# Kernel optimization log

Measured on AMD Instinct MI355X. Metric: run time of the kernel, lower is better.

Reference implementation:

```python
import jax, jax.numpy as jnp
import numpy as np

N = 100_000   # nodes
D = 128       # in_size == out_size
E = 800_000   # edges per etype
NE = 2        # number of edge types
H = 4         # num_heads
HD = D // H   # head size
EPS = 1e-5


def setup_inputs() -> dict:
    key = jax.random.key(0)
    ks = jax.random.split(key, 10)
    s = 0.05
    return {
        "feat": jax.random.normal(ks[0], (N, D), jnp.float32),
        "src": jax.random.randint(ks[1], (NE, E), 0, N, dtype=jnp.int32),
        "dst": jax.random.randint(ks[2], (NE, E), 0, N, dtype=jnp.int32),
        # per-etype Linear weights stored [in, out] so y = x @ W + b (torch stores transposed)
        "Wt": jax.random.normal(ks[3], (NE, D, D), jnp.float32) * s,
        "bt": jnp.zeros((NE, D), jnp.float32),
        "Kw": jax.random.normal(ks[4], (NE, D, D), jnp.float32) * s,
        "Kb": jnp.zeros((NE, D), jnp.float32),
        "Qw": jax.random.normal(ks[5], (NE, D, D), jnp.float32) * s,
        "Qb": jnp.zeros((NE, D), jnp.float32),
        "Vw": jax.random.normal(ks[6], (NE, D, D), jnp.float32) * s,
        "Vb": jnp.zeros((NE, D), jnp.float32),
        "ln_g": jnp.ones((D,), jnp.float32),
        "ln_b": jnp.zeros((D,), jnp.float32),
    }


def _attn(Wh, kw, kb, qw, qb, vw, vb):
    # per-node multi-head attention ACROSS HEADS: attn is [N, H, H] (faithful to bmm in torch code)
    k = (Wh @ kw + kb).reshape(-1, H, HD)
    q = (Wh @ qw + qb).reshape(-1, H, HD)
    v = (Wh @ vw + vb).reshape(-1, H, HD)
    scores = jnp.einsum('nhd,ngd->nhg', q, k) / np.float32(np.sqrt(HD))
    a = jax.nn.softmax(scores, axis=2)  # dropout is identity in eval
    return jnp.einsum('nhg,ngd->nhd', a, v).reshape(-1, D)


def reference(feat, src, dst, Wt, bt, Kw, Kb, Qw, Qb, Vw, Vb, ln_g, ln_b):
    h = jnp.zeros_like(feat)
    ones_e = jnp.ones((E,), feat.dtype)
    for e in range(NE):  # small fixed loop over edge types
        Wh = _attn(feat @ Wt[e] + bt[e], Kw[e], Kb[e], Qw[e], Qb[e], Vw[e], Vb[e])
        msg = Wh[src[e]]                                      # copy_u: [E, D]
        tot = jax.ops.segment_sum(msg, dst[e], num_segments=N)
        deg = jax.ops.segment_sum(ones_e, dst[e], num_segments=N)
        h = h + tot / jnp.maximum(deg, 1.0)[:, None]          # mean (0 for isolated), cross-etype 'sum'
    h = h + feat  # identity residual (in_size == out_size)
    mu = jnp.mean(h, axis=-1, keepdims=True)
    var = jnp.mean((h - mu) ** 2, axis=-1, keepdims=True)
    return (h - mu) / jnp.sqrt(var + EPS) * ln_g + ln_b  # LayerNorm; dropout identity in eval
```

## Files before the change

### kernel.cpp

```cpp
#include <hip/hip_runtime.h>
#include <hip/hip_bf16.h>
#include <stdint.h>

#define D 128
#define NET 2
#define CAP 32
#define CSTR 4
#define NB_BUILD 128

typedef __bf16 bf16x8 __attribute__((ext_vector_type(8)));
typedef float f32x4 __attribute__((ext_vector_type(4)));
typedef short s16x8 __attribute__((ext_vector_type(8)));
typedef unsigned short us16x8 __attribute__((ext_vector_type(8)));

__device__ __forceinline__ float b2f(unsigned short u) {
  return __builtin_bit_cast(float, ((uint32_t)u) << 16);
}
__device__ __forceinline__ unsigned short f2b(float f) {
  __hip_bfloat16 h = __float2bfloat16(f);
  return __builtin_bit_cast(unsigned short, h);
}

__global__ void k_combine(const float* __restrict__ Wt, const float* __restrict__ bt,
                          const float* __restrict__ Kw, const float* __restrict__ Kb,
                          const float* __restrict__ Qw, const float* __restrict__ Qb,
                          const float* __restrict__ Vw, const float* __restrict__ Vb,
                          unsigned short* __restrict__ WTc, float* __restrict__ bc) {
  int combo = blockIdx.y;
  int et = combo / 3, which = combo % 3;
  const float* W0 = Wt + (size_t)et * D * D;
  const float* W1 = ((which == 0) ? Kw : (which == 1) ? Qw : Vw) + (size_t)et * D * D;
  const float* b1 = ((which == 0) ? Kb : (which == 1) ? Qb : Vb) + (size_t)et * D;
  const float* b0 = bt + (size_t)et * D;

  int t = threadIdx.x;
  int i = blockIdx.x * 16 + (t >> 4);
  int jb = (t & 15) * 8;
  float acc[8];
#pragma unroll
  for (int j = 0; j < 8; j++) acc[j] = 0.f;
  for (int k = 0; k < D; k++) {
    float a0 = W0[(size_t)i * D + k];
    const float* w1p = W1 + (size_t)k * D + jb;
#pragma unroll
    for (int j = 0; j < 8; j++) acc[j] += a0 * w1p[j];
  }
  unsigned short* wout = WTc + (size_t)combo * D * D;
#pragma unroll
  for (int j = 0; j < 8; j++) wout[(size_t)(jb + j) * D + i] = f2b(acc[j]);

  if (blockIdx.x == 0 && t < D) {
    float s = b1[t];
    for (int k = 0; k < D; k++) s += b0[k] * W1[(size_t)k * D + t];
    bc[(size_t)combo * D + t] = s;
  }
}

__device__ __forceinline__ void stage_w(const unsigned short* __restrict__ W,
                                        unsigned short (*Ws)[136], int tid) {
  int r = tid >> 1, hh = tid & 1;
  const us16x8* gp = (const us16x8*)(W + (size_t)r * D + hh * 64);
  us16x8* lp = (us16x8*)&Ws[r][hh * 64];
#pragma unroll
  for (int i = 0; i < 8; i++) lp[i] = gp[i];
}

__device__ __forceinline__ void load_pf(const unsigned short* __restrict__ W,
                                        us16x8* pf, int sr, int sh) {
  const us16x8* gp = (const us16x8*)(W + (size_t)sr * D + sh * 64);
#pragma unroll
  for (int i = 0; i < 8; i++) pf[i] = gp[i];
}

__device__ __forceinline__ void write_pf(const us16x8* pf, unsigned short (*Ws)[136],
                                         int sr, int sh) {
  us16x8* lp = (us16x8*)&Ws[sr][sh * 64];
#pragma unroll
  for (int i = 0; i < 8; i++) lp[i] = pf[i];
}

__device__ __forceinline__ void gemm_frag(const bf16x8* af, unsigned short (*Ws)[136],
                                          int m, int q, f32x4* acc) {
#pragma unroll
  for (int nt = 0; nt < 8; nt++) {
    f32x4 a = {0.f, 0.f, 0.f, 0.f};
#pragma unroll
    for (int ks = 0; ks < 4; ks++) {
      s16x8 br = *(const s16x8*)&Ws[nt * 16 + m][ks * 32 + q * 8];
      a = __builtin_amdgcn_mfma_f32_16x16x32_bf16(af[ks], __builtin_bit_cast(bf16x8, br), a, 0, 0, 0);
    }
    acc[nt] = a;
  }
}

__global__ __launch_bounds__(256) void k_fused(
    const float* __restrict__ feat, const unsigned short* __restrict__ WTc,
    const float* __restrict__ bc, unsigned short* __restrict__ Whall, int nrows,
    const int* __restrict__ src, const int* __restrict__ dst,
    int* __restrict__ cnt, int* __restrict__ bucket, int Eper) {
  __shared__ unsigned short As[64][136];
  __shared__ unsigned short Ws[128][136];
  int tid = threadIdx.x;
  int bid = blockIdx.x;

  if (bid < NB_BUILD) {
    int nE2 = NET * Eper;
    int chunk = (nE2 + NB_BUILD - 1) / NB_BUILD;
    int start = bid * chunk;
    int end = start + chunk; if (end > nE2) end = nE2;
    for (int j = start; j < end; j += 2048) {
      int idx[8]; int dd[8]; int ss[8]; bool vld[8];
#pragma unroll
      for (int u = 0; u < 8; u++) {
        idx[u] = j + (u << 8) + tid;
        vld[u] = idx[u] < end;
        int jj = vld[u] ? idx[u] : start;
        dd[u] = dst[jj];
        ss[u] = src[jj];
      }
      int key[8]; int slot[8];
#pragma unroll
      for (int u = 0; u < 8; u++) {
        int et = (idx[u] >= Eper) ? 1 : 0;
        key[u] = et * nrows + dd[u];
        slot[u] = CAP;
        if (vld[u]) slot[u] = atomicAdd(&cnt[(size_t)key[u] * CSTR], 1);
      }
#pragma unroll
      for (int u = 0; u < 8; u++) {
        int et = (idx[u] >= Eper) ? 1 : 0;
        if (vld[u] && slot[u] < CAP)
          bucket[(size_t)key[u] * CAP + slot[u]] = ss[u] + et * nrows;
      }
    }
    return;
  }

  int id = bid - NB_BUILD;
  int row0 = id * 64;
  int w = tid >> 6, lane = tid & 63;
  int m = lane & 15, q = lane >> 4;

  {
    int r = tid >> 2, qq = tid & 3;
    int gr = row0 + r;
    unsigned short tmp[32];
    if (gr < nrows) {
      const f32x4* gp = (const f32x4*)(feat + (size_t)gr * D + qq * 32);
#pragma unroll
      for (int i = 0; i < 8; i++) {
        f32x4 v = gp[i];
#pragma unroll
        for (int j = 0; j < 4; j++) tmp[i * 4 + j] = f2b(v[j]);
      }
    } else {
#pragma unroll
      for (int i = 0; i < 32; i++) tmp[i] = 0;
    }
    us16x8* lp = (us16x8*)&As[r][qq * 32];
#pragma unroll
    for (int i = 0; i < 4; i++) lp[i] = *(const us16x8*)&tmp[i * 8];
  }
  stage_w(WTc, Ws, tid);
  __syncthreads();

  bf16x8 af[4];
#pragma unroll
  for (int ks = 0; ks < 4; ks++)
    af[ks] = __builtin_bit_cast(bf16x8, *(const s16x8*)&As[w * 16 + m][ks * 32 + q * 8]);

  int sr = tid >> 1, sh = tid & 1;
  us16x8 pf[8];
  load_pf(WTc + (size_t)1 * D * D, pf, sr, sh);

  const float scale = 0.17677669529663687f;

#pragma unroll
  for (int et = 0; et < NET; et++) {
    f32x4 acc[3][8];
#pragma unroll
    for (int which = 0; which < 3; which++) {
      const int combo = et * 3 + which;
      gemm_frag(af, Ws, m, q, acc[which]);
      const float* bb = bc + (size_t)combo * D;
#pragma unroll
      for (int nt = 0; nt < 8; nt++) acc[which][nt] += bb[nt * 16 + m];
      if (combo < 5) {
        __syncthreads();
        write_pf(pf, Ws, sr, sh);
        if (combo < 4)
          load_pf(WTc + (size_t)(combo + 2) * D * D, pf, sr, sh);
        __syncthreads();
      }
    }

    f32x4* kacc = acc[0];
    f32x4* qacc = acc[1];
    f32x4* vacc = acc[2];
    unsigned short* Wh = Whall + (size_t)et * nrows * D;
#pragma unroll
    for (int r = 0; r < 4; r++) {
      float sc[4][4];
#pragma unroll
      for (int hh = 0; hh < 4; hh++)
#pragma unroll
        for (int gg = 0; gg < 4; gg++)
          sc[hh][gg] = qacc[2 * hh][r] * kacc[2 * gg][r] + qacc[2 * hh + 1][r] * kacc[2 * gg + 1][r];
#pragma unroll
      for (int off = 1; off < 16; off <<= 1)
#pragma unroll
        for (int hh = 0; hh < 4; hh++)
#pragma unroll
          for (int gg = 0; gg < 4; gg++)
            sc[hh][gg] += __shfl_xor(sc[hh][gg], off, 64);
      float a[4][4];
#pragma unroll
      for (int hh = 0; hh < 4; hh++) {
        float s0 = sc[hh][0] * scale, s1 = sc[hh][1] * scale;
        float s2 = sc[hh][2] * scale, s3 = sc[hh][3] * scale;
        float mx = fmaxf(fmaxf(s0, s1), fmaxf(s2, s3));
        float e0 = __expf(s0 - mx), e1 = __expf(s1 - mx);
        float e2 = __expf(s2 - mx), e3 = __expf(s3 - mx);
        float inv = 1.f / (e0 + e1 + e2 + e3);
        a[hh][0] = e0 * inv; a[hh][1] = e1 * inv; a[hh][2] = e2 * inv; a[hh][3] = e3 * inv;
      }
      int grow = row0 + w * 16 + q * 4 + r;
      if (grow < nrows) {
        unsigned short* op = Wh + (size_t)grow * D;
#pragma unroll
        for (int nt = 0; nt < 8; nt++) {
          int hh = nt >> 1, lo = nt & 1;
          float o = a[hh][0] * vacc[0 + lo][r] + a[hh][1] * vacc[2 + lo][r] +
                    a[hh][2] * vacc[4 + lo][r] + a[hh][3] * vacc[6 + lo][r];
          op[nt * 16 + m] = f2b(o);
        }
      }
    }
  }
}

__global__ __launch_bounds__(256) void k_gather_ln(
    const unsigned short* __restrict__ Whall, const int* __restrict__ bucket,
    const int* __restrict__ cnt, const float* __restrict__ feat,
    const float* __restrict__ g, const float* __restrict__ b,
    float* __restrict__ out, int n) {
  int lane = threadIdx.x & 63, wv = threadIdx.x >> 6;
  int node = blockIdx.x * 4 + wv;
  if (node >= n) return;

  int c0 = cnt[(size_t)node * CSTR], c1 = cnt[(size_t)(n + node) * CSTR];
  int c0c = min(c0, CAP), c1c = min(c1, CAP);
  float w0 = 1.0f / fmaxf((float)c0, 1.0f);
  float w1 = 1.0f / fmaxf((float)c1, 1.0f);

  const float2* fp = (const float2*)(feat + (size_t)node * D);
  float2 fv = fp[lane];

  int myid = 0;
  if (lane < 32) {
    if (lane < c0c) myid = bucket[(size_t)node * CAP + lane];
  } else {
    if (lane - 32 < c1c) myid = bucket[((size_t)n + node) * CAP + (lane - 32)];
  }

  float a0 = 0.f, a1 = 0.f;
  for (int j = 0; j < c0c; j += 8) {
    int sid[8]; float wt[8];
#pragma unroll
    for (int u = 0; u < 8; u++) {
      int jj = j + u;
      bool v = jj < c0c;
      sid[u] = __shfl(myid, v ? jj : 0, 64);
      wt[u] = v ? w0 : 0.f;
    }
    ushort2 vv[8];
#pragma unroll
    for (int u = 0; u < 8; u++)
      vv[u] = *(const ushort2*)(Whall + (size_t)sid[u] * D + 2 * lane);
#pragma unroll
    for (int u = 0; u < 8; u++) {
      a0 += wt[u] * b2f(vv[u].x);
      a1 += wt[u] * b2f(vv[u].y);
    }
  }
  for (int j = 0; j < c1c; j += 8) {
    int sid[8]; float wt[8];
#pragma unroll
    for (int u = 0; u < 8; u++) {
      int jj = j + u;
      bool v = jj < c1c;
      sid[u] = __shfl(myid, v ? 32 + jj : 32, 64);
      wt[u] = v ? w1 : 0.f;
    }
    ushort2 vv[8];
#pragma unroll
    for (int u = 0; u < 8; u++)
      vv[u] = *(const ushort2*)(Whall + (size_t)sid[u] * D + 2 * lane);
#pragma unroll
    for (int u = 0; u < 8; u++) {
      a0 += wt[u] * b2f(vv[u].x);
      a1 += wt[u] * b2f(vv[u].y);
    }
  }

  float x0 = a0 + fv.x;
  float x1 = a1 + fv.y;

  float s = x0 + x1, s2 = x0 * x0 + x1 * x1;
#pragma unroll
  for (int off = 32; off > 0; off >>= 1) {
    s += __shfl_xor(s, off, 64);
    s2 += __shfl_xor(s2, off, 64);
  }
  float mu = s * (1.0f / 128.0f);
  float var = fmaxf(s2 * (1.0f / 128.0f) - mu * mu, 0.0f);
  float rs = rsqrtf(var + 1e-5f);

  float2 gv = ((const float2*)g)[lane];
  float2 bv = ((const float2*)b)[lane];
  float2 ov;
  ov.x = (x0 - mu) * rs * gv.x + bv.x;
  ov.y = (x1 - mu) * rs * gv.y + bv.y;
  ((float2*)(out + (size_t)node * D))[lane] = ov;
}

extern "C" void kernel_launch(void* const* d_in, const int* in_sizes, int n_in,
                              void* d_out, int out_size, void* d_ws, size_t ws_size,
                              hipStream_t stream) {
  const float* feat = (const float*)d_in[0];
  const int* src = (const int*)d_in[1];
  const int* dst = (const int*)d_in[2];
  const float* Wt = (const float*)d_in[3];
  const float* bt = (const float*)d_in[4];
  const float* Kw = (const float*)d_in[5];
  const float* Kb = (const float*)d_in[6];
  const float* Qw = (const float*)d_in[7];
  const float* Qb = (const float*)d_in[8];
  const float* Vw = (const float*)d_in[9];
  const float* Vb = (const float*)d_in[10];
  const float* lng = (const float*)d_in[11];
  const float* lnb = (const float*)d_in[12];

  const int N = in_sizes[0] / D;
  const int E = in_sizes[1] / NET;

  char* p = (char*)d_ws;
  unsigned short* Whall = (unsigned short*)p;  p += (size_t)NET * N * D * 2;
  int* bucket = (int*)p;                       p += (size_t)NET * N * CAP * sizeof(int);
  int* cnt = (int*)p;                          p += (size_t)NET * N * CSTR * sizeof(int);
  unsigned short* WTc = (unsigned short*)p;    p += (size_t)NET * 3 * D * D * 2;
  float* bc = (float*)p;

  hipMemsetAsync(cnt, 0, (size_t)NET * N * CSTR * sizeof(int), stream);
  k_combine<<<dim3(8, NET * 3), 256, 0, stream>>>(Wt, bt, Kw, Kb, Qw, Qb, Vw, Vb, WTc, bc);

  int ng = (N + 63) / 64;
  k_fused<<<NB_BUILD + ng, 256, 0, stream>>>(feat, WTc, bc, Whall, N, src, dst, cnt, bucket, E);

  k_gather_ln<<<(N + 3) / 4, 256, 0, stream>>>(Whall, bucket, cnt, feat, lng, lnb,
                                               (float*)d_out, N);
}
```

Measured before the change: 337.1 us.

## Split wavefront into half-waves gathering alternate edges with 8-byte loads

The gather/LayerNorm kernel now merges both edge-type loops into a single loop over the combined neighbor list. Each half-wavefront handles alternate edges and loads 4 bf16 values per lane instead of 2. The two halves' partial sums are then combined with a cross-half shuffle, and the LayerNorm reduction runs over 32 lanes. This is meant to cut loop overhead and tail waste from two separately padded loops and to use wider loads per row, at the cost of extra shuffles and half the lanes sitting idle on the final store.

```diff
diff --git a/kernel.cpp b/kernel.cpp
--- a/kernel.cpp
+++ b/kernel.cpp
@@ -12,6 +12,7 @@
 typedef float f32x4 __attribute__((ext_vector_type(4)));
 typedef short s16x8 __attribute__((ext_vector_type(8)));
 typedef unsigned short us16x8 __attribute__((ext_vector_type(8)));
+typedef unsigned short us16x4 __attribute__((ext_vector_type(4)));
 
 __device__ __forceinline__ float b2f(unsigned short u) {
   return __builtin_bit_cast(float, ((uint32_t)u) << 16);
@@ -247,14 +248,16 @@
   int lane = threadIdx.x & 63, wv = threadIdx.x >> 6;
   int node = blockIdx.x * 4 + wv;
   if (node >= n) return;
+  int hw = lane >> 5;
+  int hl = lane & 31;
 
   int c0 = cnt[(size_t)node * CSTR], c1 = cnt[(size_t)(n + node) * CSTR];
   int c0c = min(c0, CAP), c1c = min(c1, CAP);
+  int ce = c0c + c1c;
   float w0 = 1.0f / fmaxf((float)c0, 1.0f);
   float w1 = 1.0f / fmaxf((float)c1, 1.0f);
 
-  const float2* fp = (const float2*)(feat + (size_t)node * D);
-  float2 fv = fp[lane];
+  f32x4 fv = ((const f32x4*)(feat + (size_t)node * D))[hl];
 
   int myid = 0;
   if (lane < 32) {
@@ -263,52 +266,44 @@
     if (lane - 32 < c1c) myid = bucket[((size_t)n + node) * CAP + (lane - 32)];
   }
 
-  float a0 = 0.f, a1 = 0.f;
-  for (int j = 0; j < c0c; j += 8) {
+  float a0 = 0.f, a1 = 0.f, a2 = 0.f, a3 = 0.f;
+  for (int base = 0; base < ce; base += 16) {
     int sid[8]; float wt[8];
 #pragma unroll
     for (int u = 0; u < 8; u++) {
-      int jj = j + u;
-      bool v = jj < c0c;
-      sid[u] = __shfl(myid, v ? jj : 0, 64);
-      wt[u] = v ? w0 : 0.f;
-    }
-    ushort2 vv[8];
+      int k = base + 2 * u + hw;
+      bool v = k < ce;
+      bool is0 = k < c0c;
+      int sidx = v ? (is0 ? k : k - c0c + 32) : 0;
+      sid[u] = __shfl(myid, sidx, 64);
+      wt[u] = v ? (is0 ? w0 : w1) : 0.f;
+    }
+    us16x4 vv[8];
 #pragma unroll
     for (int u = 0; u < 8; u++)
-      vv[u] = *(const ushort2*)(Whall + (size_t)sid[u] * D + 2 * lane);
+      vv[u] = *(const us16x4*)(Whall + (size_t)sid[u] * D + hl * 4);
 #pragma unroll
     for (int u = 0; u < 8; u++) {
       a0 += wt[u] * b2f(vv[u].x);
       a1 += wt[u] * b2f(vv[u].y);
-    }
-  }
-  for (int j = 0; j < c1c; j += 8) {
-    int sid[8]; float wt[8];
-#pragma unroll
-    for (int u = 0; u < 8; u++) {
-      int jj = j + u;
-      bool v = jj < c1c;
-      sid[u] = __shfl(myid, v ? 32 + jj : 32, 64);
-      wt[u] = v ? w1 : 0.f;
-    }
-    ushort2 vv[8];
-#pragma unroll
-    for (int u = 0; u < 8; u++)
-      vv[u] = *(const ushort2*)(Whall + (size_t)sid[u] * D + 2 * lane);
-#pragma unroll
-    for (int u = 0; u < 8; u++) {
-      a0 += wt[u] * b2f(vv[u].x);
-      a1 += wt[u] * b2f(vv[u].y);
-    }
-  }
+      a2 += wt[u] * b2f(vv[u].z);
+      a3 += wt[u] * b2f(vv[u].w);
+    }
+  }
+  a0 += __shfl_xor(a0, 32, 64);
+  a1 += __shfl_xor(a1, 32, 64);
+  a2 += __shfl_xor(a2, 32, 64);
+  a3 += __shfl_xor(a3, 32, 64);
 
   float x0 = a0 + fv.x;
   float x1 = a1 + fv.y;
-
-  float s = x0 + x1, s2 = x0 * x0 + x1 * x1;
-#pragma unroll
-  for (int off = 32; off > 0; off >>= 1) {
+  float x2 = a2 + fv.z;
+  float x3 = a3 + fv.w;
+
+  float s = x0 + x1 + x2 + x3;
+  float s2 = x0 * x0 + x1 * x1 + x2 * x2 + x3 * x3;
+#pragma unroll
+  for (int off = 16; off > 0; off >>= 1) {
     s += __shfl_xor(s, off, 64);
     s2 += __shfl_xor(s2, off, 64);
   }
@@ -316,12 +311,16 @@
   float var = fmaxf(s2 * (1.0f / 128.0f) - mu * mu, 0.0f);
   float rs = rsqrtf(var + 1e-5f);
 
-  float2 gv = ((const float2*)g)[lane];
-  float2 bv = ((const float2*)b)[lane];
-  float2 ov;
-  ov.x = (x0 - mu) * rs * gv.x + bv.x;
-  ov.y = (x1 - mu) * rs * gv.y + bv.y;
-  ((float2*)(out + (size_t)node * D))[lane] = ov;
+  if (lane < 32) {
+    f32x4 gv = ((const f32x4*)g)[hl];
+    f32x4 bv = ((const f32x4*)b)[hl];
+    f32x4 ov;
+    ov.x = (x0 - mu) * rs * gv.x + bv.x;
+    ov.y = (x1 - mu) * rs * gv.y + bv.y;
+    ov.z = (x2 - mu) * rs * gv.z + bv.z;
+    ov.w = (x3 - mu) * rs * gv.w + bv.w;
+    ((f32x4*)(out + (size_t)node * D))[hl] = ov;
+  }
 }
 
 extern "C" void kernel_launch(void* const* d_in, const int* in_sizes, int n_in,
```

Result: slower. 345.6 us (+2.5%).

## Load A fragments directly from global, fold count memset into combine kernel

Applied to the files above, without the earlier changes.

The A operand is now loaded straight from feat into MFMA fragment registers, which removes the As shared-memory tile and its LDS round trip. Dropping As cuts shared memory per block, and the launch bounds now ask for 4 blocks per CU to raise occupancy. The separate hipMemsetAsync on the count array is replaced by a zeroing loop inside k_combine, saving one launch. The zeroing runs on only 48 blocks, so the memset may be slow, and the direct global loads are less coalesced than the old staged copy.

```diff
diff --git a/kernel.cpp b/kernel.cpp
--- a/kernel.cpp
+++ b/kernel.cpp
@@ -25,7 +25,18 @@
                           const float* __restrict__ Kw, const float* __restrict__ Kb,
                           const float* __restrict__ Qw, const float* __restrict__ Qb,
                           const float* __restrict__ Vw, const float* __restrict__ Vb,
-                          unsigned short* __restrict__ WTc, float* __restrict__ bc) {
+                          unsigned short* __restrict__ WTc, float* __restrict__ bc,
+                          int* __restrict__ cnt, int ncnt) {
+  int t = threadIdx.x;
+  {
+    int4* c4 = (int4*)cnt;
+    int n4 = ncnt >> 2;
+    int gid = (blockIdx.y * gridDim.x + blockIdx.x) * 256 + t;
+    int gsz = gridDim.x * gridDim.y * 256;
+    const int4 z = {0, 0, 0, 0};
+    for (int i = gid; i < n4; i += gsz) c4[i] = z;
+  }
+
   int combo = blockIdx.y;
   int et = combo / 3, which = combo % 3;
   const float* W0 = Wt + (size_t)et * D * D;
@@ -33,7 +44,6 @@
   const float* b1 = ((which == 0) ? Kb : (which == 1) ? Qb : Vb) + (size_t)et * D;
   const float* b0 = bt + (size_t)et * D;
 
-  int t = threadIdx.x;
   int i = blockIdx.x * 16 + (t >> 4);
   int jb = (t & 15) * 8;
   float acc[8];
@@ -93,12 +103,11 @@
   }
 }
 
-__global__ __launch_bounds__(256) void k_fused(
+__global__ __launch_bounds__(256, 4) void k_fused(
     const float* __restrict__ feat, const unsigned short* __restrict__ WTc,
     const float* __restrict__ bc, unsigned short* __restrict__ Whall, int nrows,
     const int* __restrict__ src, const int* __restrict__ dst,
     int* __restrict__ cnt, int* __restrict__ bucket, int Eper) {
-  __shared__ unsigned short As[64][136];
   __shared__ unsigned short Ws[128][136];
   int tid = threadIdx.x;
   int bid = blockIdx.x;
@@ -140,34 +149,31 @@
   int row0 = id * 64;
   int w = tid >> 6, lane = tid & 63;
   int m = lane & 15, q = lane >> 4;
-
+  int grow_a = row0 + w * 16 + m;
+
+  bf16x8 af[4];
   {
-    int r = tid >> 2, qq = tid & 3;
-    int gr = row0 + r;
-    unsigned short tmp[32];
-    if (gr < nrows) {
-      const f32x4* gp = (const f32x4*)(feat + (size_t)gr * D + qq * 32);
-#pragma unroll
-      for (int i = 0; i < 8; i++) {
-        f32x4 v = gp[i];
-#pragma unroll
-        for (int j = 0; j < 4; j++) tmp[i * 4 + j] = f2b(v[j]);
-      }
-    } else {
-#pragma unroll
-      for (int i = 0; i < 32; i++) tmp[i] = 0;
-    }
-    us16x8* lp = (us16x8*)&As[r][qq * 32];
-#pragma unroll
-    for (int i = 0; i < 4; i++) lp[i] = *(const us16x8*)&tmp[i * 8];
+    bool vr = grow_a < nrows;
+    const float* fr = feat + (size_t)(vr ? grow_a : 0) * D + q * 8;
+    f32x4 lo[4], hi[4];
+#pragma unroll
+    for (int ks = 0; ks < 4; ks++) {
+      lo[ks] = *(const f32x4*)(fr + ks * 32);
+      hi[ks] = *(const f32x4*)(fr + ks * 32 + 4);
+    }
+#pragma unroll
+    for (int ks = 0; ks < 4; ks++) {
+      unsigned short t[8];
+#pragma unroll
+      for (int j = 0; j < 4; j++) {
+        t[j] = f2b(vr ? lo[ks][j] : 0.f);
+        t[4 + j] = f2b(vr ? hi[ks][j] : 0.f);
+      }
+      af[ks] = __builtin_bit_cast(bf16x8, *(const s16x8*)t);
+    }
   }
   stage_w(WTc, Ws, tid);
   __syncthreads();
-
-  bf16x8 af[4];
-#pragma unroll
-  for (int ks = 0; ks < 4; ks++)
-    af[ks] = __builtin_bit_cast(bf16x8, *(const s16x8*)&As[w * 16 + m][ks * 32 + q * 8]);
 
   int sr = tid >> 1, sh = tid & 1;
   us16x8 pf[8];
@@ -229,9 +235,9 @@
         unsigned short* op = Wh + (size_t)grow * D;
 #pragma unroll
         for (int nt = 0; nt < 8; nt++) {
-          int hh = nt >> 1, lo = nt & 1;
-          float o = a[hh][0] * vacc[0 + lo][r] + a[hh][1] * vacc[2 + lo][r] +
-                    a[hh][2] * vacc[4 + lo][r] + a[hh][3] * vacc[6 + lo][r];
+          int hh = nt >> 1, lo2 = nt & 1;
+          float o = a[hh][0] * vacc[0 + lo2][r] + a[hh][1] * vacc[2 + lo2][r] +
+                    a[hh][2] * vacc[4 + lo2][r] + a[hh][3] * vacc[6 + lo2][r];
           op[nt * 16 + m] = f2b(o);
         }
       }
@@ -351,8 +357,9 @@
   unsigned short* WTc = (unsigned short*)p;    p += (size_t)NET * 3 * D * D * 2;
   float* bc = (float*)p;
 
-  hipMemsetAsync(cnt, 0, (size_t)NET * N * CSTR * sizeof(int), stream);
-  k_combine<<<dim3(8, NET * 3), 256, 0, stream>>>(Wt, bt, Kw, Kb, Qw, Qb, Vw, Vb, WTc, bc);
+  int ncnt = NET * N * CSTR;
+  k_combine<<<dim3(8, NET * 3), 256, 0, stream>>>(Wt, bt, Kw, Kb, Qw, Qb, Vw, Vb, WTc, bc,
+                                                  cnt, ncnt);
 
   int ng = (N + 63) / 64;
   k_fused<<<NB_BUILD + ng, 256, 0, stream>>>(feat, WTc, bc, Whall, N, src, dst, cnt, bucket, E);
```

Result: slower. 487.7 us (+44.7%).
